# Kernel optimization log

Hardware: AMD Instinct MI355X
Metric: run time of the kernel (lower is better)

## Reference

```python
import jax, jax.numpy as jnp
import numpy as np

H = 1024  # hidden size
T = 4096  # sequence length


def setup_inputs() -> dict:
    key = jax.random.key(0)
    ks = jax.random.split(key, 11)
    s = 1.0 / np.sqrt(H)  # torch LSTM/Linear default init scale
    u = lambda k, shape: jax.random.uniform(k, shape, jnp.float32, -s, s)
    return {
        "x": jax.random.normal(ks[0], (1, T, 2), jnp.float32),
        # layer 0 (input size 2)
        "W_ih0": u(ks[1], (4 * H, 2)),
        "W_hh0": u(ks[2], (4 * H, H)),
        "b_ih0": u(ks[3], (4 * H,)),
        "b_hh0": u(ks[4], (4 * H,)),
        # layers 1-2 (input size H), stacked
        "W_ih12": u(ks[5], (2, 4 * H, H)),
        "W_hh12": u(ks[6], (2, 4 * H, H)),
        "b_ih12": u(ks[7], (2, 4 * H)),
        "b_hh12": u(ks[8], (2, 4 * H)),
        # output head Linear(H, 1)
        "W_res": u(ks[9], (1, H)),
        "b_res": u(ks[10], (1,)),
    }


def reference(x, W_ih0, W_hh0, b_ih0, b_hh0, W_ih12, W_hh12, b_ih12, b_hh12, W_res, b_res):
    xs = x[0]  # (T, 2); BATCH == 1
    W_ihs = [W_ih0, W_ih12[0], W_ih12[1]]
    W_hhs = [W_hh0, W_hh12[0], W_hh12[1]]
    b_ihs = [b_ih0, b_ih12[0], b_ih12[1]]
    b_hhs = [b_hh0, b_hh12[0], b_hh12[1]]

    def cell(inp, h, c, W_ih, W_hh, b_ih, b_hh):
        # PyTorch gate order: input, forget, cell(g), output
        gates = W_ih @ inp + b_ih + W_hh @ h + b_hh  # (4H,)
        i, f, g, o = jnp.split(gates, 4)
        i = jax.nn.sigmoid(i)
        f = jax.nn.sigmoid(f)
        g = jnp.tanh(g)
        o = jax.nn.sigmoid(o)
        c_new = f * c + i * g
        h_new = o * jnp.tanh(c_new)
        return h_new, c_new

    def step(carry, x_t):
        h, c = carry  # each (3, H)
        inp = x_t
        hs, cs = [], []
        for l in range(3):  # fixed small layer loop
            h_new, c_new = cell(inp, h[l], c[l], W_ihs[l], W_hhs[l], b_ihs[l], b_hhs[l])
            hs.append(h_new)
            cs.append(c_new)
            inp = h_new
        return (jnp.stack(hs), jnp.stack(cs)), inp  # emit top-layer h

    h0 = jnp.zeros((3, H), x.dtype)
    c0 = jnp.zeros((3, H), x.dtype)
    _, ys = jax.lax.scan(step, (h0, c0), xs)  # ys: (T, H)
    y = jax.nn.sigmoid(ys @ W_res.T + b_res)  # (T, 1)
    return y.reshape(1, T)
```

## Files before the change

### kernel.cpp

```cpp
#include <hip/hip_runtime.h>

#define HSZ 1024
#define TSTEPS 4096
#define NBLK 256
#define NTHR 256
#define HV (HSZ / 4)
#define REP_BYTES 24576

typedef _Float16 half2v __attribute__((ext_vector_type(2)));

#if __has_builtin(__builtin_amdgcn_fdot2)
#define FDOT2(a, b, c) __builtin_amdgcn_fdot2((a), (b), (c), false)
#else
__device__ __forceinline__ float FDOT2(half2v a, half2v b, float c) {
    return c + (float)a.x * (float)b.x + (float)a.y * (float)b.y;
}
#endif

__device__ __forceinline__ int f2i(float f) { int i; __builtin_memcpy(&i, &f, 4); return i; }
__device__ __forceinline__ float i2f(int i) { float f; __builtin_memcpy(&f, &i, 4); return f; }

template <int CTRL, int RM>
__device__ __forceinline__ float dpp_acc(float v) {
    int t = __builtin_amdgcn_update_dpp(0, f2i(v), CTRL, RM, 0xf, true);
    return v + i2f(t);
}
__device__ __forceinline__ float wave_sum63(float v) {
    v = dpp_acc<0x111, 0xf>(v);
    v = dpp_acc<0x112, 0xf>(v);
    v = dpp_acc<0x114, 0xf>(v);
    v = dpp_acc<0x118, 0xf>(v);
    v = dpp_acc<0x142, 0xa>(v);
    v = dpp_acc<0x143, 0xc>(v);
    return v;
}

__device__ __forceinline__ float sigm(float x) { return 1.0f / (1.0f + __expf(-x)); }
__device__ __forceinline__ float tanh_fast(float x) {
    const float e = __expf(2.0f * x);
    return 1.0f - 2.0f / (e + 1.0f);
}

__device__ __forceinline__ unsigned long long ld_coh64(const unsigned long long* p) {
    return __hip_atomic_load(p, __ATOMIC_RELAXED, __HIP_MEMORY_SCOPE_AGENT);
}
__device__ __forceinline__ void st_coh32(unsigned* p, unsigned v) {
    __hip_atomic_store(p, v, __ATOMIC_RELAXED, __HIP_MEMORY_SCOPE_AGENT);
}

__device__ __forceinline__ unsigned f16bits(float v) {
    _Float16 h = (_Float16)v;
    unsigned short b;
    __builtin_memcpy(&b, &h, 2);
    return (unsigned)b;
}

#define PINH(h) asm volatile("" : "+v"(h))

__device__ __forceinline__ half2v cvt2(float a, float b) {
    half2v r; r.x = (_Float16)a; r.y = (_Float16)b; return r;
}

__device__ __forceinline__ half2v unpk(unsigned long long q) {
    const unsigned v = ((unsigned)q & 0xFFFFu) | ((unsigned)(q >> 32) << 16);
    half2v h; __builtin_memcpy(&h, &v, 4); return h;
}

struct PollA { unsigned long long q[8]; };

__device__ __forceinline__ PollA poll_issueA(const unsigned long long* A, int lane) {
    PollA p;
#pragma unroll
    for (int i = 0; i < 4; ++i) {
        p.q[2 * i]     = ld_coh64(A + 2 * lane + 128 * i);
        p.q[2 * i + 1] = ld_coh64(A + 2 * lane + 128 * i + 1);
    }
    return p;
}

__device__ __forceinline__ void poll_completeA(PollA& p, const unsigned long long* A,
                                               unsigned e, int lane, half2v* hf) {
    const unsigned long long K =
        ((unsigned long long)e << 16) | ((unsigned long long)e << 48);
    for (;;) {
        unsigned long long bad = 0;
#pragma unroll
        for (int j = 0; j < 8; ++j) bad |= (p.q[j] ^ K);
        bad &= 0xFFFF0000FFFF0000ull;
        if (__all(bad == 0)) break;
        __builtin_amdgcn_s_sleep(1);
#pragma unroll
        for (int i = 0; i < 4; ++i) {
            p.q[2 * i]     = ld_coh64(A + 2 * lane + 128 * i);
            p.q[2 * i + 1] = ld_coh64(A + 2 * lane + 128 * i + 1);
        }
    }
#pragma unroll
    for (int j = 0; j < 8; ++j) hf[j] = unpk(p.q[j]);
}

__global__ void __launch_bounds__(NTHR, 1) lstm_persist(
    const float* __restrict__ x,
    const float* __restrict__ Wih0, const float* __restrict__ Whh0,
    const float* __restrict__ bih0, const float* __restrict__ bhh0,
    const float* __restrict__ Wih12, const float* __restrict__ Whh12,
    const float* __restrict__ bih12, const float* __restrict__ bhh12,
    const float* __restrict__ Wres, const float* __restrict__ bres,
    float* __restrict__ out, float* __restrict__ ws_f, int nrep)
{
    char* wsb = (char*)ws_f;
    const int lane = threadIdx.x & 63;
    const int u = blockIdx.x * (NTHR / 64) + (threadIdx.x >> 6);
    const int tid = threadIdx.x;

    {
        const int gid = blockIdx.x * NTHR + tid;
        if (gid < nrep * 3072) {
            const int rep = gid / 3072, d = gid % 3072;
            st_coh32((unsigned*)(wsb + rep * REP_BYTES) + 3072 + d, 0u);
        }
    }

    float b0[4], b1[4], b2[4], wx0a[4], wx0b[4];
#pragma unroll
    for (int g = 0; g < 4; ++g) {
        const int r = g * HSZ + u;
        b0[g] = bih0[r] + bhh0[r];
        b1[g] = bih12[r] + bhh12[r];
        b2[g] = bih12[4 * HSZ + r] + bhh12[4 * HSZ + r];
        wx0a[g] = Wih0[2 * r];
        wx0b[g] = Wih0[2 * r + 1];
    }

    const float4* Whh0v = (const float4*)Whh0;
    const float4* Wih1v = (const float4*)Wih12;
    const float4* Whh1v = (const float4*)Whh12;
    const float4* Wih2v = (const float4*)(Wih12 + 4 * HSZ * HSZ);
    const float4* Whh2v = (const float4*)(Whh12 + 4 * HSZ * HSZ);

    half2v w0h[4][8], wi1h[4][8], wh1h[4][8], wi2h[4][8], wh2h[4][8];
#pragma unroll
    for (int g = 0; g < 4; ++g) {
        const size_t r = (size_t)(g * HSZ + u) * HV + lane;
#pragma unroll
        for (int i = 0; i < 4; ++i) {
            float4 t;
            t = Whh0v[r + 64 * i];  w0h[g][2*i] = cvt2(t.x,t.y);  w0h[g][2*i+1] = cvt2(t.z,t.w);
            t = Wih1v[r + 64 * i];  wi1h[g][2*i] = cvt2(t.x,t.y); wi1h[g][2*i+1] = cvt2(t.z,t.w);
            t = Whh1v[r + 64 * i];  wh1h[g][2*i] = cvt2(t.x,t.y); wh1h[g][2*i+1] = cvt2(t.z,t.w);
            t = Wih2v[r + 64 * i];  wi2h[g][2*i] = cvt2(t.x,t.y); wi2h[g][2*i+1] = cvt2(t.z,t.w);
            t = Whh2v[r + 64 * i];  wh2h[g][2*i] = cvt2(t.x,t.y); wh2h[g][2*i+1] = cvt2(t.z,t.w);
        }
    }
#pragma unroll
    for (int g = 0; g < 4; ++g)
#pragma unroll
        for (int j = 0; j < 8; ++j) {
            PINH(w0h[g][j]); PINH(wi1h[g][j]); PINH(wh1h[g][j]);
            PINH(wi2h[g][j]); PINH(wh2h[g][j]);
        }

    half2v wresh[8];
    {
        const float4* wr = (const float4*)Wres;
#pragma unroll
        for (int i = 0; i < 4; ++i) {
            float4 t = wr[lane + 64 * i];
            wresh[2*i] = cvt2(t.x, t.y); wresh[2*i+1] = cvt2(t.z, t.w);
        }
    }
    const float bres0 = bres[0];

    asm volatile("s_waitcnt vmcnt(0)" ::: "memory");
    __syncthreads();

    const unsigned long long* Tmyq =
        (const unsigned long long*)(wsb + (blockIdx.x % nrep) * REP_BYTES);

    float c0 = 0.0f, c1 = 0.0f, c2 = 0.0f;

    PollA pq0 = poll_issueA(Tmyq + 1536, lane);

    for (int k = 0; k <= TSTEPS + 2; ++k) {
        const int wp = k & 1, rp = wp ^ 1;
        const unsigned e = (unsigned)k;
        const unsigned long long* Trp = Tmyq + rp * 1536;
        const unsigned long long* Tnx = Tmyq + wp * 1536;
        const bool pub = (k <= TSTEPS + 1);
        const unsigned tg = (unsigned)(k + 1) << 16;

        half2v haf[8];
        poll_completeA(pq0, Trp, e, lane, haf);
        PollA pq1 = poll_issueA(Trp + 512, lane);

        float h0v = 0.0f;
        if (k < TSTEPS) {
            const float x0 = x[2 * k], x1 = x[2 * k + 1];
            float acc[4];
#pragma unroll
            for (int g = 0; g < 4; ++g) {
                float a = 0.0f;
#pragma unroll
                for (int j = 0; j < 8; ++j) a = FDOT2(w0h[g][j], haf[j], a);
                acc[g] = a;
            }
#pragma unroll
            for (int g = 0; g < 4; ++g) acc[g] = wave_sum63(acc[g]);
            if (lane == 63) {
                const float ig = sigm(acc[0] + b0[0] + wx0a[0] * x0 + wx0b[0] * x1);
                const float fg = sigm(acc[1] + b0[1] + wx0a[1] * x0 + wx0b[1] * x1);
                const float gg = tanh_fast(acc[2] + b0[2] + wx0a[2] * x0 + wx0b[2] * x1);
                const float og = sigm(acc[3] + b0[3] + wx0a[3] * x0 + wx0b[3] * x1);
                c0 = fg * c0 + ig * gg;
                h0v = og * tanh_fast(c0);
            }
        }
        if (lane == 63 && pub) {
            const unsigned wb = tg | f16bits(h0v);
            for (int rep = 0; rep < nrep; ++rep)
                st_coh32((unsigned*)(wsb + rep * REP_BYTES) + wp * 3072 + u, wb);
        }

        half2v hbf[8];
        poll_completeA(pq1, Trp + 512, e, lane, hbf);
        PollA pq2 = poll_issueA(Trp + 1024, lane);

        float h1v = 0.0f;
        if (k >= 1 && k <= TSTEPS) {
            float acc[4];
#pragma unroll
            for (int g = 0; g < 4; ++g) {
                float a = 0.0f;
#pragma unroll
                for (int j = 0; j < 8; ++j) {
                    a = FDOT2(wi1h[g][j], haf[j], a);
                    a = FDOT2(wh1h[g][j], hbf[j], a);
                }
                acc[g] = a;
            }
#pragma unroll
            for (int g = 0; g < 4; ++g) acc[g] = wave_sum63(acc[g]);
            if (lane == 63) {
                const float ig = sigm(acc[0] + b1[0]);
                const float fg = sigm(acc[1] + b1[1]);
                const float gg = tanh_fast(acc[2] + b1[2]);
                const float og = sigm(acc[3] + b1[3]);
                c1 = fg * c1 + ig * gg;
                h1v = og * tanh_fast(c1);
            }
        }
        if (lane == 63 && pub) {
            const unsigned wb = tg | f16bits(h1v);
            for (int rep = 0; rep < nrep; ++rep)
                st_coh32((unsigned*)(wsb + rep * REP_BYTES) + wp * 3072 + 1024 + u, wb);
        }

        half2v hcf[8];
        poll_completeA(pq2, Trp + 1024, e, lane, hcf);
        pq0 = poll_issueA(Tnx, lane);

        if (u == 0 && k >= 3) {
            float a = 0.0f;
#pragma unroll
            for (int j = 0; j < 8; ++j) a = FDOT2(wresh[j], hcf[j], a);
            a = wave_sum63(a);
            if (lane == 63) out[k - 3] = sigm(a + bres0);
        }

        float h2v = 0.0f;
        if (k >= 2 && k <= TSTEPS + 1) {
            float acc[4];
#pragma unroll
            for (int g = 0; g < 4; ++g) {
                float a = 0.0f;
#pragma unroll
                for (int j = 0; j < 8; ++j) {
                    a = FDOT2(wi2h[g][j], hbf[j], a);
                    a = FDOT2(wh2h[g][j], hcf[j], a);
                }
                acc[g] = a;
            }
#pragma unroll
            for (int g = 0; g < 4; ++g) acc[g] = wave_sum63(acc[g]);
            if (lane == 63) {
                const float ig = sigm(acc[0] + b2[0]);
                const float fg = sigm(acc[1] + b2[1]);
                const float gg = tanh_fast(acc[2] + b2[2]);
                const float og = sigm(acc[3] + b2[3]);
                c2 = fg * c2 + ig * gg;
                h2v = og * tanh_fast(c2);
            }
        }
        if (lane == 63 && pub) {
            const unsigned wb = tg | f16bits(h2v);
            for (int rep = 0; rep < nrep; ++rep)
                st_coh32((unsigned*)(wsb + rep * REP_BYTES) + wp * 3072 + 2048 + u, wb);
        }
    }
}

extern "C" void kernel_launch(void* const* d_in, const int* in_sizes, int n_in,
                              void* d_out, int out_size, void* d_ws, size_t ws_size,
                              hipStream_t stream) {
    const float* x     = (const float*)d_in[0];
    const float* Wih0  = (const float*)d_in[1];
    const float* Whh0  = (const float*)d_in[2];
    const float* bih0  = (const float*)d_in[3];
    const float* bhh0  = (const float*)d_in[4];
    const float* Wih12 = (const float*)d_in[5];
    const float* Whh12 = (const float*)d_in[6];
    const float* bih12 = (const float*)d_in[7];
    const float* bhh12 = (const float*)d_in[8];
    const float* Wres  = (const float*)d_in[9];
    const float* bres  = (const float*)d_in[10];
    float* out = (float*)d_out;
    float* ws  = (float*)d_ws;

    int nrep = (int)(ws_size / REP_BYTES);
    if (nrep > 8) nrep = 8;
    if (nrep < 1) nrep = 1;

    lstm_persist<<<dim3(NBLK), dim3(NTHR), 0, stream>>>(
        x, Wih0, Whh0, bih0, bhh0, Wih12, Whh12, bih12, bhh12,
        Wres, bres, out, ws, nrep);
}
```

Baseline: 14.05 ms.

## Poll global hidden state with one wave per layer and share via LDS

Instead of every wave in a block polling the coherent global exchange buffer for all three layer vectors, one designated wave per layer polls global memory and republishes the payload into double-buffered LDS with a workgroup-scope flag. The other waves spin on the LDS flag and read from shared memory. A v_perm builtin also replaces the shift/mask unpacking, and the output head moves to after the layer-2 publish. This cuts global/L2 polling traffic by roughly four times, at the cost of an extra LDS hop and intra-block spin latency on the critical path.

```diff
diff --git a/kernel.cpp b/kernel.cpp
--- a/kernel.cpp
+++ b/kernel.cpp
@@ -61,9 +61,16 @@
     half2v r; r.x = (_Float16)a; r.y = (_Float16)b; return r;
 }
 
-__device__ __forceinline__ half2v unpk(unsigned long long q) {
-    const unsigned v = ((unsigned)q & 0xFFFFu) | ((unsigned)(q >> 32) << 16);
+__device__ __forceinline__ half2v bits_to_h2(unsigned v) {
     half2v h; __builtin_memcpy(&h, &v, 4); return h;
+}
+
+__device__ __forceinline__ unsigned pack_payload(unsigned long long q) {
+#if __has_builtin(__builtin_amdgcn_perm)
+    return __builtin_amdgcn_perm((unsigned)(q >> 32), (unsigned)q, 0x05040100u);
+#else
+    return ((unsigned)q & 0xFFFFu) | ((unsigned)(q >> 32) << 16);
+#endif
 }
 
 struct PollA { unsigned long long q[8]; };
@@ -79,7 +86,7 @@
 }
 
 __device__ __forceinline__ void poll_completeA(PollA& p, const unsigned long long* A,
-                                               unsigned e, int lane, half2v* hf) {
+                                               unsigned e, int lane, unsigned* pay) {
     const unsigned long long K =
         ((unsigned long long)e << 16) | ((unsigned long long)e << 48);
     for (;;) {
@@ -96,7 +103,32 @@
         }
     }
 #pragma unroll
-    for (int j = 0; j < 8; ++j) hf[j] = unpk(p.q[j]);
+    for (int j = 0; j < 8; ++j) pay[j] = pack_payload(p.q[j]);
+}
+
+__device__ __forceinline__ void lds_publish(unsigned* payrow, unsigned* flag,
+                                            const unsigned* pay, unsigned e, int lane) {
+    uint2* P = (uint2*)payrow;
+#pragma unroll
+    for (int i = 0; i < 4; ++i) {
+        uint2 t; t.x = pay[2 * i]; t.y = pay[2 * i + 1];
+        P[lane + 64 * i] = t;
+    }
+    asm volatile("s_waitcnt lgkmcnt(0)" ::: "memory");
+    __hip_atomic_store(flag, e, __ATOMIC_RELAXED, __HIP_MEMORY_SCOPE_WORKGROUP);
+}
+
+__device__ __forceinline__ void lds_consume(const unsigned* payrow, const unsigned* flag,
+                                            unsigned e, int lane, half2v* hf) {
+    while (__hip_atomic_load(flag, __ATOMIC_RELAXED, __HIP_MEMORY_SCOPE_WORKGROUP) != e) {}
+    asm volatile("" ::: "memory");
+    const uint2* P = (const uint2*)payrow;
+#pragma unroll
+    for (int i = 0; i < 4; ++i) {
+        uint2 t = P[lane + 64 * i];
+        hf[2 * i]     = bits_to_h2(t.x);
+        hf[2 * i + 1] = bits_to_h2(t.y);
+    }
 }
 
 __global__ void __launch_bounds__(NTHR, 1) lstm_persist(
@@ -110,8 +142,12 @@
 {
     char* wsb = (char*)ws_f;
     const int lane = threadIdx.x & 63;
-    const int u = blockIdx.x * (NTHR / 64) + (threadIdx.x >> 6);
+    const int wid = threadIdx.x >> 6;
+    const int u = blockIdx.x * (NTHR / 64) + wid;
     const int tid = threadIdx.x;
+
+    __shared__ __align__(16) unsigned lds_pay[2][3][512];
+    __shared__ unsigned lds_flag[2][3];
 
     {
         const int gid = blockIdx.x * NTHR + tid;
@@ -119,6 +155,7 @@
             const int rep = gid / 3072, d = gid % 3072;
             st_coh32((unsigned*)(wsb + rep * REP_BYTES) + 3072 + d, 0u);
         }
+        if (tid < 6) ((unsigned*)lds_flag)[tid] = 0xFFFFFFFFu;
     }
 
     float b0[4], b1[4], b2[4], wx0a[4], wx0b[4];
@@ -179,19 +216,29 @@
 
     float c0 = 0.0f, c1 = 0.0f, c2 = 0.0f;
 
-    PollA pq0 = poll_issueA(Tmyq + 1536, lane);
+    PollA pq0;
+    if (wid == 0) pq0 = poll_issueA(Tmyq + 1536, lane);
 
     for (int k = 0; k <= TSTEPS + 2; ++k) {
-        const int wp = k & 1, rp = wp ^ 1;
+        const int wp = k & 1, rp = wp ^ 1, lp = k & 1;
         const unsigned e = (unsigned)k;
         const unsigned long long* Trp = Tmyq + rp * 1536;
         const unsigned long long* Tnx = Tmyq + wp * 1536;
         const bool pub = (k <= TSTEPS + 1);
         const unsigned tg = (unsigned)(k + 1) << 16;
+        PollA pq1, pq2;
 
         half2v haf[8];
-        poll_completeA(pq0, Trp, e, lane, haf);
-        PollA pq1 = poll_issueA(Trp + 512, lane);
+        if (wid == 0) {
+            unsigned pay[8];
+            poll_completeA(pq0, Trp, e, lane, pay);
+            lds_publish(&lds_pay[lp][0][0], &lds_flag[lp][0], pay, e, lane);
+#pragma unroll
+            for (int j = 0; j < 8; ++j) haf[j] = bits_to_h2(pay[j]);
+        } else {
+            lds_consume(&lds_pay[lp][0][0], &lds_flag[lp][0], e, lane, haf);
+        }
+        if (wid == 1) pq1 = poll_issueA(Trp + 512, lane);
 
         float h0v = 0.0f;
         if (k < TSTEPS) {
@@ -222,8 +269,16 @@
         }
 
         half2v hbf[8];
-        poll_completeA(pq1, Trp + 512, e, lane, hbf);
-        PollA pq2 = poll_issueA(Trp + 1024, lane);
+        if (wid == 1) {
+            unsigned pay[8];
+            poll_completeA(pq1, Trp + 512, e, lane, pay);
+            lds_publish(&lds_pay[lp][1][0], &lds_flag[lp][1], pay, e, lane);
+#pragma unroll
+            for (int j = 0; j < 8; ++j) hbf[j] = bits_to_h2(pay[j]);
+        } else {
+            lds_consume(&lds_pay[lp][1][0], &lds_flag[lp][1], e, lane, hbf);
+        }
+        if (wid == 2) pq2 = poll_issueA(Trp + 1024, lane);
 
         float h1v = 0.0f;
         if (k >= 1 && k <= TSTEPS) {
@@ -256,16 +311,16 @@
         }
 
         half2v hcf[8];
-        poll_completeA(pq2, Trp + 1024, e, lane, hcf);
-        pq0 = poll_issueA(Tnx, lane);
-
-        if (u == 0 && k >= 3) {
-            float a = 0.0f;
-#pragma unroll
-            for (int j = 0; j < 8; ++j) a = FDOT2(wresh[j], hcf[j], a);
-            a = wave_sum63(a);
-            if (lane == 63) out[k - 3] = sigm(a + bres0);
-        }
+        if (wid == 2) {
+            unsigned pay[8];
+            poll_completeA(pq2, Trp + 1024, e, lane, pay);
+            lds_publish(&lds_pay[lp][2][0], &lds_flag[lp][2], pay, e, lane);
+#pragma unroll
+            for (int j = 0; j < 8; ++j) hcf[j] = bits_to_h2(pay[j]);
+        } else {
+            lds_consume(&lds_pay[lp][2][0], &lds_flag[lp][2], e, lane, hcf);
+        }
+        if (wid == 0) pq0 = poll_issueA(Tnx, lane);
 
         float h2v = 0.0f;
         if (k >= 2 && k <= TSTEPS + 1) {
@@ -295,6 +350,14 @@
             const unsigned wb = tg | f16bits(h2v);
             for (int rep = 0; rep < nrep; ++rep)
                 st_coh32((unsigned*)(wsb + rep * REP_BYTES) + wp * 3072 + 2048 + u, wb);
+        }
+
+        if (u == 0 && k >= 3) {
+            float a = 0.0f;
+#pragma unroll
+            for (int j = 0; j < 8; ++j) a = FDOT2(wresh[j], hcf[j], a);
+            a = wave_sum63(a);
+            if (lane == 63) out[k - 3] = sigm(a + bres0);
         }
     }
 }
```

New measurement: 15.98 ms. +13.7%, slower.

## Poll all three layer states up front and prefetch next-step buffers early

Applied to the files above, without the earlier changes.

The kernel now completes the polls for all three layers' previous hidden states at the top of each step, instead of interleaving them with compute. It then issues the next step's polls immediately after each layer publishes, so the loads for the following step are in flight during the remaining compute. The x load is hoisted before the polls, unpacking uses a v_perm byte permute, and the output head moves to the end of the step. This removes per-layer poll stalls in the middle of a step, at the cost of one combined wait at the start and more live registers.

```diff
diff --git a/kernel.cpp b/kernel.cpp
--- a/kernel.cpp
+++ b/kernel.cpp
@@ -61,9 +61,16 @@
     half2v r; r.x = (_Float16)a; r.y = (_Float16)b; return r;
 }
 
-__device__ __forceinline__ half2v unpk(unsigned long long q) {
-    const unsigned v = ((unsigned)q & 0xFFFFu) | ((unsigned)(q >> 32) << 16);
+__device__ __forceinline__ half2v bits_to_h2(unsigned v) {
     half2v h; __builtin_memcpy(&h, &v, 4); return h;
+}
+
+__device__ __forceinline__ unsigned pack_payload(unsigned long long q) {
+#if __has_builtin(__builtin_amdgcn_perm)
+    return __builtin_amdgcn_perm((unsigned)(q >> 32), (unsigned)q, 0x05040100u);
+#else
+    return ((unsigned)q & 0xFFFFu) | ((unsigned)(q >> 32) << 16);
+#endif
 }
 
 struct PollA { unsigned long long q[8]; };
@@ -96,7 +103,7 @@
         }
     }
 #pragma unroll
-    for (int j = 0; j < 8; ++j) hf[j] = unpk(p.q[j]);
+    for (int j = 0; j < 8; ++j) hf[j] = bits_to_h2(pack_payload(p.q[j]));
 }
 
 __global__ void __launch_bounds__(NTHR, 1) lstm_persist(
@@ -179,7 +186,9 @@
 
     float c0 = 0.0f, c1 = 0.0f, c2 = 0.0f;
 
-    PollA pq0 = poll_issueA(Tmyq + 1536, lane);
+    PollA pa0 = poll_issueA(Tmyq + 1536, lane);
+    PollA pa1 = poll_issueA(Tmyq + 1536 + 512, lane);
+    PollA pa2 = poll_issueA(Tmyq + 1536 + 1024, lane);
 
     for (int k = 0; k <= TSTEPS + 2; ++k) {
         const int wp = k & 1, rp = wp ^ 1;
@@ -189,13 +198,16 @@
         const bool pub = (k <= TSTEPS + 1);
         const unsigned tg = (unsigned)(k + 1) << 16;
 
-        half2v haf[8];
-        poll_completeA(pq0, Trp, e, lane, haf);
-        PollA pq1 = poll_issueA(Trp + 512, lane);
+        float x0 = 0.0f, x1 = 0.0f;
+        if (k < TSTEPS) { x0 = x[2 * k]; x1 = x[2 * k + 1]; }
+
+        half2v haf[8], hbf[8], hcf[8];
+        poll_completeA(pa0, Trp, e, lane, haf);
+        poll_completeA(pa1, Trp + 512, e, lane, hbf);
+        poll_completeA(pa2, Trp + 1024, e, lane, hcf);
 
         float h0v = 0.0f;
         if (k < TSTEPS) {
-            const float x0 = x[2 * k], x1 = x[2 * k + 1];
             float acc[4];
 #pragma unroll
             for (int g = 0; g < 4; ++g) {
@@ -220,10 +232,7 @@
             for (int rep = 0; rep < nrep; ++rep)
                 st_coh32((unsigned*)(wsb + rep * REP_BYTES) + wp * 3072 + u, wb);
         }
-
-        half2v hbf[8];
-        poll_completeA(pq1, Trp + 512, e, lane, hbf);
-        PollA pq2 = poll_issueA(Trp + 1024, lane);
+        pa0 = poll_issueA(Tnx, lane);
 
         float h1v = 0.0f;
         if (k >= 1 && k <= TSTEPS) {
@@ -254,18 +263,7 @@
             for (int rep = 0; rep < nrep; ++rep)
                 st_coh32((unsigned*)(wsb + rep * REP_BYTES) + wp * 3072 + 1024 + u, wb);
         }
-
-        half2v hcf[8];
-        poll_completeA(pq2, Trp + 1024, e, lane, hcf);
-        pq0 = poll_issueA(Tnx, lane);
-
-        if (u == 0 && k >= 3) {
-            float a = 0.0f;
-#pragma unroll
-            for (int j = 0; j < 8; ++j) a = FDOT2(wresh[j], hcf[j], a);
-            a = wave_sum63(a);
-            if (lane == 63) out[k - 3] = sigm(a + bres0);
-        }
+        pa1 = poll_issueA(Tnx + 512, lane);
 
         float h2v = 0.0f;
         if (k >= 2 && k <= TSTEPS + 1) {
@@ -295,6 +293,15 @@
             const unsigned wb = tg | f16bits(h2v);
             for (int rep = 0; rep < nrep; ++rep)
                 st_coh32((unsigned*)(wsb + rep * REP_BYTES) + wp * 3072 + 2048 + u, wb);
+        }
+        pa2 = poll_issueA(Tnx + 1024, lane);
+
+        if (u == 0 && k >= 3) {
+            float a = 0.0f;
+#pragma unroll
+            for (int j = 0; j < 8; ++j) a = FDOT2(wresh[j], hcf[j], a);
+            a = wave_sum63(a);
+            if (lane == 63) out[k - 3] = sigm(a + bres0);
         }
     }
 }
```

Result: slower. 46.46 ms (+230.6%).
